# Performance work log

Measured on AMD Instinct MI355X. Metric: run time of the kernel, lower is better.

## Reference

```python
import jax, jax.numpy as jnp
import numpy as np

NUM_GRAPHS = 512
EPS_BN = 1e-5


def _bn(x, g, b):
    # BatchNorm1d in training mode: biased batch statistics over node dim
    m = x.mean(0)
    v = x.var(0)
    return g * (x - m) * jax.lax.rsqrt(v + EPS_BN) + b


def _gcn(x, W, b, src, dst):
    # GCNConv with self-loops and symmetric deg^-1/2 normalization
    n = x.shape[0]
    loop = jnp.arange(n, dtype=src.dtype)
    s = jnp.concatenate([src, loop])
    d = jnp.concatenate([dst, loop])
    h = x @ W  # [N, C_out]
    deg = jax.ops.segment_sum(jnp.ones(d.shape[0], dtype=h.dtype), d, num_segments=n)
    dinv = jax.lax.rsqrt(jnp.maximum(deg, 1.0))  # deg >= 1 due to self-loops
    norm = dinv[s] * dinv[d]  # [E+N]
    out = jax.ops.segment_sum(norm[:, None] * h[s], d, num_segments=n)
    return out + b


def setup_inputs() -> dict:
    key = jax.random.key(0)
    ks = jax.random.split(key, 16)
    N, E, F = 100000, 1600000, 6

    def lin(k, fi, fo):
        k1, k2 = jax.random.split(k)
        s = 1.0 / np.sqrt(fi)
        return (jax.random.uniform(k1, (fi, fo), minval=-s, maxval=s),
                jax.random.uniform(k2, (fo,), minval=-s, maxval=s))

    W1, b1 = lin(ks[0], F, 32)
    W2, b2 = lin(ks[1], 32, 64)
    W3, b3 = lin(ks[2], 64, 128)
    Wf1, bf1 = lin(ks[3], 128, 128)
    Wf2, bf2 = lin(ks[4], 128, 64)
    return {
        "x": jax.random.normal(ks[5], (N, F), dtype=jnp.float32),
        "edge_src": jax.random.randint(ks[6], (E,), 0, N, dtype=jnp.int32),
        "edge_dst": jax.random.randint(ks[7], (E,), 0, N, dtype=jnp.int32),
        "batch": jnp.sort(jax.random.randint(ks[8], (N,), 0, NUM_GRAPHS, dtype=jnp.int32)),
        "W1": W1, "b1": b1, "g1": jnp.ones(32), "be1": jnp.zeros(32),
        "W2": W2, "b2": b2, "g2": jnp.ones(64), "be2": jnp.zeros(64),
        "W3": W3, "b3": b3, "g3": jnp.ones(128), "be3": jnp.zeros(128),
        "Wf1": Wf1, "bf1": bf1, "g4": jnp.ones(128), "be4": jnp.zeros(128),
        "Wf2": Wf2, "bf2": bf2,
    }


def reference(x, edge_src, edge_dst, batch,
              W1, b1, g1, be1, W2, b2, g2, be2, W3, b3, g3, be3,
              Wf1, bf1, g4, be4, Wf2, bf2):
    h = jax.nn.relu(_bn(_gcn(x, W1, b1, edge_src, edge_dst), g1, be1))
    h = jax.nn.relu(_bn(_gcn(h, W2, b2, edge_src, edge_dst), g2, be2))
    h = jax.nn.relu(_bn(_gcn(h, W3, b3, edge_src, edge_dst), g3, be3))
    p = jax.ops.segment_max(h, batch, num_segments=NUM_GRAPHS)  # [G, 128]
    p = jax.nn.relu(_bn(p @ Wf1 + bf1, g4, be4))  # dropout = identity (eval)
    p = p @ Wf2 + bf2
    return p / jnp.maximum(jnp.linalg.norm(p, axis=1, keepdims=True), 1e-12)
```

## Files before the change

kernel.cpp:

```cpp
#include <hip/hip_runtime.h>
#include <hip/hip_bf16.h>
#include <hip/hip_fp16.h>

#define NG 512
#define EPS_BN 1e-5f

typedef unsigned short ushort_t;
typedef unsigned int uint_t;

__device__ __forceinline__ float4 f4add(float4 a, float4 b) {
    a.x += b.x; a.y += b.y; a.z += b.z; a.w += b.w; return a;
}
__device__ __forceinline__ float4 f4fma(float s, float4 b, float4 a) {
    a.x = fmaf(s, b.x, a.x); a.y = fmaf(s, b.y, a.y);
    a.z = fmaf(s, b.z, a.z); a.w = fmaf(s, b.w, a.w); return a;
}
__device__ __forceinline__ float4 f4scale(float s, float4 a) {
    a.x *= s; a.y *= s; a.z *= s; a.w *= s; return a;
}
__device__ __forceinline__ float4 bnrelu4(float4 v, float4 sc, float4 sh) {
    float4 r;
    r.x = fmaxf(fmaf(sc.x, v.x, sh.x), 0.f);
    r.y = fmaxf(fmaf(sc.y, v.y, sh.y), 0.f);
    r.z = fmaxf(fmaf(sc.z, v.z, sh.z), 0.f);
    r.w = fmaxf(fmaf(sc.w, v.w, sh.w), 0.f);
    return r;
}
__device__ __forceinline__ void bnparam(float sm, float sq, float ga, float bt,
                                        float invN, float& sc, float& sh) {
    float m = sm * invN;
    float var = fmaf(-m, m, sq * invN);
    sc = ga * rsqrtf(var + EPS_BN);
    sh = fmaf(-m, sc, bt);
}

__device__ __forceinline__ float4 ldh4(const ushort_t* p) {
    uint2 u = *reinterpret_cast<const uint2*>(p);
    __half2 a = *reinterpret_cast<const __half2*>(&u.x);
    __half2 b = *reinterpret_cast<const __half2*>(&u.y);
    float2 fa = __half22float2(a), fb = __half22float2(b);
    float4 r; r.x = fa.x; r.y = fa.y; r.z = fb.x; r.w = fb.y; return r;
}
__device__ __forceinline__ void sth4(ushort_t* p, float4 v) {
    __half2 a = __float22half2_rn(make_float2(v.x, v.y));
    __half2 b = __float22half2_rn(make_float2(v.z, v.w));
    uint2 u;
    u.x = *reinterpret_cast<uint_t*>(&a);
    u.y = *reinterpret_cast<uint_t*>(&b);
    *reinterpret_cast<uint2*>(p) = u;
}


__global__ void k_count(const int* __restrict__ dst, int* __restrict__ cnt, int E) {
    int i = blockIdx.x * blockDim.x + threadIdx.x;
    if (i < E) atomicAdd(&cnt[dst[i]], 1);
}

__global__ void k_dinv(const int* __restrict__ cnt, float* __restrict__ dinv, int N) {
    int i = blockIdx.x * blockDim.x + threadIdx.x;
    if (i < N) dinv[i] = rsqrtf((float)cnt[i] + 1.0f);
}


#define SCAN_T 256
#define SCAN_I 4

__global__ void k_scan1(const int* __restrict__ in, int* __restrict__ out,
                        int* __restrict__ bsum, int N) {
    __shared__ int lds[SCAN_T];
    int t = threadIdx.x;
    int base = blockIdx.x * (SCAN_T * SCAN_I) + t * SCAN_I;
    int v[SCAN_I];
    int sum = 0;
#pragma unroll
    for (int i = 0; i < SCAN_I; ++i) {
        int idx = base + i;
        v[i] = (idx < N) ? in[idx] : 0;
        sum += v[i];
    }
    lds[t] = sum;
    __syncthreads();
    for (int o = 1; o < SCAN_T; o <<= 1) {
        int a = (t >= o) ? lds[t - o] : 0;
        __syncthreads();
        lds[t] += a;
        __syncthreads();
    }
    int run = lds[t] - sum;
#pragma unroll
    for (int i = 0; i < SCAN_I; ++i) {
        int idx = base + i;
        if (idx < N) out[idx] = run;
        run += v[i];
    }
    if (t == SCAN_T - 1) bsum[blockIdx.x] = lds[SCAN_T - 1];
}

__global__ void k_scan2(int* __restrict__ bs, int nb) {
    __shared__ int lds[SCAN_T];
    int t = threadIdx.x;
    int runbase = 0;
    for (int start = 0; start < nb; start += SCAN_T) {
        int idx = start + t;
        int v = (idx < nb) ? bs[idx] : 0;
        lds[t] = v;
        __syncthreads();
        for (int o = 1; o < SCAN_T; o <<= 1) {
            int a = (t >= o) ? lds[t - o] : 0;
            __syncthreads();
            lds[t] += a;
            __syncthreads();
        }
        if (idx < nb) bs[idx] = runbase + lds[t] - v;
        int tot = lds[SCAN_T - 1];
        __syncthreads();
        runbase += tot;
    }
}

__global__ void k_scan3(int* __restrict__ out, const int* __restrict__ bs, int N) {
    int add = bs[blockIdx.x];
    int base = blockIdx.x * (SCAN_T * SCAN_I) + threadIdx.x * SCAN_I;
#pragma unroll
    for (int i = 0; i < SCAN_I; ++i) {
        int idx = base + i;
        if (idx < N) out[idx] += add;
    }
}


__global__ void k_bucket(const int* __restrict__ src, const int* __restrict__ dst,
                         const float* __restrict__ dinv, const int* __restrict__ rowptr,
                         int* __restrict__ fill, int2* __restrict__ e2, int E) {
    int e = blockIdx.x * blockDim.x + threadIdx.x;
    if (e >= E) return;
    int d = dst[e], s = src[e];
    int pos = rowptr[d] + atomicAdd(&fill[d], 1);
    e2[pos] = make_int2(s, __float_as_int(dinv[s]));
}


template <int COUT>
__global__ __launch_bounds__(256) void k_layer1(
    const int* __restrict__ rowptr, const int* __restrict__ cnt,
    const int2* __restrict__ e2, const float* __restrict__ dinv,
    const float* __restrict__ x, const float* __restrict__ W,
    ushort_t* __restrict__ hout, float* __restrict__ sums,
    float* __restrict__ sumsq, int N) {
    constexpr int NPB = 256;
    constexpr int CG = COUT / 4;
    constexpr int RPB = 256 / CG;
    constexpr int ECAP1 = 4608;
    __shared__ float inT[NPB * 6];
    __shared__ float4 wT[6 * CG];
    __shared__ float4 red[256];
    __shared__ int2 eLDS[ECAP1];
    int t = threadIdx.x;
    const float4* W4 = (const float4*)W;
    for (int i = t; i < 6 * CG; i += 256) wT[i] = W4[i];
    int base = blockIdx.x * NPB;
    int lastn = min(base + NPB, N) - 1;
    int eBeg = rowptr[base];
    int eEnd = rowptr[lastn] + cnt[lastn];
    int M = eEnd - eBeg;
    bool useL = (M <= ECAP1);
    if (useL) {
        for (int i = t; i < M; i += 256) eLDS[i] = e2[eBeg + i];
    }
    __syncthreads();
    {
        const float2* x2 = (const float2*)x;
        int ew = t & 3;
        int nl0 = t >> 2;
#pragma unroll 1
        for (int it = 0; it < 4; ++it) {
            int nl = it * 64 + nl0;
            int n = base + nl;
            float a0 = 0, a1 = 0, a2 = 0, a3 = 0, a4 = 0, a5 = 0;
            float di = 0.f;
            if (n < N) {
                di = dinv[n];
                int beg = rowptr[n], end = beg + cnt[n];
                if (ew == 0) {
                    size_t b3 = (size_t)n * 3;
                    float2 p0 = x2[b3], p1 = x2[b3 + 1], p2 = x2[b3 + 2];
                    a0 = di * p0.x; a1 = di * p0.y; a2 = di * p1.x;
                    a3 = di * p1.y; a4 = di * p2.x; a5 = di * p2.y;
                }
                if (useL) {
                    int r = beg - eBeg + ew, re = end - eBeg;
                    for (; r + 4 < re; r += 8) {
                        int2 pa = eLDS[r], pb = eLDS[r + 4];
                        size_t sa = (size_t)pa.x * 3, sb = (size_t)pb.x * 3;
                        float2 qa0 = x2[sa], qa1 = x2[sa + 1], qa2 = x2[sa + 2];
                        float2 qb0 = x2[sb], qb1 = x2[sb + 1], qb2 = x2[sb + 2];
                        __builtin_amdgcn_sched_barrier(0);
                        float wa = __int_as_float(pa.y), wb = __int_as_float(pb.y);
                        a0 = fmaf(wa, qa0.x, a0); a1 = fmaf(wa, qa0.y, a1);
                        a2 = fmaf(wa, qa1.x, a2); a3 = fmaf(wa, qa1.y, a3);
                        a4 = fmaf(wa, qa2.x, a4); a5 = fmaf(wa, qa2.y, a5);
                        a0 = fmaf(wb, qb0.x, a0); a1 = fmaf(wb, qb0.y, a1);
                        a2 = fmaf(wb, qb1.x, a2); a3 = fmaf(wb, qb1.y, a3);
                        a4 = fmaf(wb, qb2.x, a4); a5 = fmaf(wb, qb2.y, a5);
                    }
                    if (r < re) {
                        int2 pa = eLDS[r];
                        size_t sa = (size_t)pa.x * 3;
                        float2 qa0 = x2[sa], qa1 = x2[sa + 1], qa2 = x2[sa + 2];
                        float wa = __int_as_float(pa.y);
                        a0 = fmaf(wa, qa0.x, a0); a1 = fmaf(wa, qa0.y, a1);
                        a2 = fmaf(wa, qa1.x, a2); a3 = fmaf(wa, qa1.y, a3);
                        a4 = fmaf(wa, qa2.x, a4); a5 = fmaf(wa, qa2.y, a5);
                    }
                } else {
                    for (int e = beg + ew; e < end; e += 4) {
                        int2 pa = e2[e];
                        size_t sa = (size_t)pa.x * 3;
                        float2 qa0 = x2[sa], qa1 = x2[sa + 1], qa2 = x2[sa + 2];
                        float wa = __int_as_float(pa.y);
                        a0 = fmaf(wa, qa0.x, a0); a1 = fmaf(wa, qa0.y, a1);
                        a2 = fmaf(wa, qa1.x, a2); a3 = fmaf(wa, qa1.y, a3);
                        a4 = fmaf(wa, qa2.x, a4); a5 = fmaf(wa, qa2.y, a5);
                    }
                }
            }
#pragma unroll
            for (int m = 1; m < 4; m <<= 1) {
                a0 += __shfl_xor(a0, m); a1 += __shfl_xor(a1, m);
                a2 += __shfl_xor(a2, m); a3 += __shfl_xor(a3, m);
                a4 += __shfl_xor(a4, m); a5 += __shfl_xor(a5, m);
            }
            if (ew == 0 && n < N) {
                int o = nl * 6;
                inT[o + 0] = di * a0; inT[o + 1] = di * a1; inT[o + 2] = di * a2;
                inT[o + 3] = di * a3; inT[o + 4] = di * a4; inT[o + 5] = di * a5;
            }
        }
    }
    __syncthreads();
    int gi = t % CG, r0 = t / CG, c0 = gi * 4;
    int nrows = min(NPB, N - base);
    float4 s = {0, 0, 0, 0}, s2 = {0, 0, 0, 0};
    for (int r = r0; r < nrows; r += RPB) {
        const float* row = inT + r * 6;
        float4 acc = {0, 0, 0, 0};
#pragma unroll
        for (int k = 0; k < 6; ++k) acc = f4fma(row[k], wT[k * CG + gi], acc);
        sth4(hout + (size_t)(base + r) * COUT + gi * 4, acc);
        s = f4add(s, acc);
        s2.x = fmaf(acc.x, acc.x, s2.x);
        s2.y = fmaf(acc.y, acc.y, s2.y);
        s2.z = fmaf(acc.z, acc.z, s2.z);
        s2.w = fmaf(acc.w, acc.w, s2.w);
    }
    red[t] = s;
    for (int hh = RPB / 2; hh > 0; hh >>= 1) {
        __syncthreads();
        if (r0 < hh) red[t] = f4add(red[t], red[t + hh * CG]);
    }
    if (r0 == 0) {
        float4 a = red[t];
        atomicAdd(&sums[c0 + 0], a.x); atomicAdd(&sums[c0 + 1], a.y);
        atomicAdd(&sums[c0 + 2], a.z); atomicAdd(&sums[c0 + 3], a.w);
    }
    __syncthreads();
    red[t] = s2;
    for (int hh = RPB / 2; hh > 0; hh >>= 1) {
        __syncthreads();
        if (r0 < hh) red[t] = f4add(red[t], red[t + hh * CG]);
    }
    if (r0 == 0) {
        float4 b = red[t];
        atomicAdd(&sumsq[c0 + 0], b.x); atomicAdd(&sumsq[c0 + 1], b.y);
        atomicAdd(&sumsq[c0 + 2], b.z); atomicAdd(&sumsq[c0 + 3], b.w);
    }
}


template <int CIN, int COUT, int NPB>
__global__ __launch_bounds__(256, 4) void k_layer(
    const int* __restrict__ rowptr, const int* __restrict__ cnt,
    const int2* __restrict__ e2, const float* __restrict__ dinv,
    const ushort_t* __restrict__ hin,
    const float* __restrict__ sums_in, const float* __restrict__ sumsq_in,
    const float* __restrict__ gam, const float* __restrict__ bet,
    const float* __restrict__ W, ushort_t* __restrict__ hout,
    float* __restrict__ sums_out, float* __restrict__ sumsq_out,
    int N, float invN) {
    constexpr int TPN = CIN / 4;
    constexpr int PAD = TPN + 1;
    constexpr int ITER1 = NPB * TPN / 256;
    constexpr int NPI = 256 / TPN;
    constexpr int CG = COUT / 4;
    constexpr int RPB = 256 / CG;
    constexpr int ECAP = 2048;
    __shared__ float4 inT4[NPB * PAD];
    __shared__ float4 red[256];
    __shared__ int2 eLDS[ECAP];
    int t = threadIdx.x;
    const float4* W4 = (const float4*)W;
    int base = blockIdx.x * NPB;
    int lastn = min(base + NPB, N) - 1;
    int eBeg = rowptr[base];
    int eEnd = rowptr[lastn] + cnt[lastn];
    int M = eEnd - eBeg;
    bool useL = (M <= ECAP);
    if (useL) {
        for (int i = t; i < M; i += 256) eLDS[i] = e2[eBeg + i];
    }
    __syncthreads();
    {
        int c4 = t % TPN;
        float4 sm = reinterpret_cast<const float4*>(sums_in)[c4];
        float4 sq = reinterpret_cast<const float4*>(sumsq_in)[c4];
        float4 ga = reinterpret_cast<const float4*>(gam)[c4];
        float4 bt = reinterpret_cast<const float4*>(bet)[c4];
        float4 sc, sh;
        bnparam(sm.x, sq.x, ga.x, bt.x, invN, sc.x, sh.x);
        bnparam(sm.y, sq.y, ga.y, bt.y, invN, sc.y, sh.y);
        bnparam(sm.z, sq.z, ga.z, bt.z, invN, sc.z, sh.z);
        bnparam(sm.w, sq.w, ga.w, bt.w, invN, sc.w, sh.w);
        const ushort_t* hu = hin;
        int co = c4 * 4;
#pragma unroll
        for (int it = 0; it < ITER1; ++it) {
            int nl = it * NPI + t / TPN;
            int n = base + nl;
            if (n < N) {
                int beg = rowptr[n], end = beg + cnt[n];
                float di = dinv[n];
                float4 acc = f4scale(di, bnrelu4(ldh4(hu + (size_t)n * CIN + co), sc, sh));
                if (useL) {
                    int r = beg - eBeg, re = end - eBeg;
                    for (; r + 7 < re; r += 8) {
                        int2 p0 = eLDS[r],     p1 = eLDS[r + 1];
                        int2 p2_ = eLDS[r + 2], p3_ = eLDS[r + 3];
                        int2 p4 = eLDS[r + 4], p5 = eLDS[r + 5];
                        int2 p6 = eLDS[r + 6], p7 = eLDS[r + 7];
                        float4 v0 = ldh4(hu + (size_t)p0.x * CIN + co);
                        float4 v1 = ldh4(hu + (size_t)p1.x * CIN + co);
                        float4 v2 = ldh4(hu + (size_t)p2_.x * CIN + co);
                        float4 v3 = ldh4(hu + (size_t)p3_.x * CIN + co);
                        float4 v4 = ldh4(hu + (size_t)p4.x * CIN + co);
                        float4 v5 = ldh4(hu + (size_t)p5.x * CIN + co);
                        float4 v6 = ldh4(hu + (size_t)p6.x * CIN + co);
                        float4 v7 = ldh4(hu + (size_t)p7.x * CIN + co);
                        __builtin_amdgcn_sched_barrier(0);
                        acc = f4fma(__int_as_float(p0.y), bnrelu4(v0, sc, sh), acc);
                        acc = f4fma(__int_as_float(p1.y), bnrelu4(v1, sc, sh), acc);
                        acc = f4fma(__int_as_float(p2_.y), bnrelu4(v2, sc, sh), acc);
                        acc = f4fma(__int_as_float(p3_.y), bnrelu4(v3, sc, sh), acc);
                        acc = f4fma(__int_as_float(p4.y), bnrelu4(v4, sc, sh), acc);
                        acc = f4fma(__int_as_float(p5.y), bnrelu4(v5, sc, sh), acc);
                        acc = f4fma(__int_as_float(p6.y), bnrelu4(v6, sc, sh), acc);
                        acc = f4fma(__int_as_float(p7.y), bnrelu4(v7, sc, sh), acc);
                    }
                    for (; r + 3 < re; r += 4) {
                        int2 p0 = eLDS[r], p1 = eLDS[r + 1];
                        int2 p2_ = eLDS[r + 2], p3_ = eLDS[r + 3];
                        float4 v0 = ldh4(hu + (size_t)p0.x * CIN + co);
                        float4 v1 = ldh4(hu + (size_t)p1.x * CIN + co);
                        float4 v2 = ldh4(hu + (size_t)p2_.x * CIN + co);
                        float4 v3 = ldh4(hu + (size_t)p3_.x * CIN + co);
                        __builtin_amdgcn_sched_barrier(0);
                        acc = f4fma(__int_as_float(p0.y), bnrelu4(v0, sc, sh), acc);
                        acc = f4fma(__int_as_float(p1.y), bnrelu4(v1, sc, sh), acc);
                        acc = f4fma(__int_as_float(p2_.y), bnrelu4(v2, sc, sh), acc);
                        acc = f4fma(__int_as_float(p3_.y), bnrelu4(v3, sc, sh), acc);
                    }
                    for (; r < re; ++r) {
                        int2 p0 = eLDS[r];
                        acc = f4fma(__int_as_float(p0.y),
                                    bnrelu4(ldh4(hu + (size_t)p0.x * CIN + co), sc, sh), acc);
                    }
                } else {
                    for (int e = beg; e < end; ++e) {
                        int2 p0 = e2[e];
                        acc = f4fma(__int_as_float(p0.y),
                                    bnrelu4(ldh4(hu + (size_t)p0.x * CIN + co), sc, sh), acc);
                    }
                }
                inT4[nl * PAD + c4] = f4scale(di, acc);
            }
        }
    }
    __syncthreads();
    int gi = t % CG, r0 = t / CG, c0 = gi * 4;
    int nrows = min(NPB, N - base);
    float4 s = {0, 0, 0, 0}, s2 = {0, 0, 0, 0};
    for (int r = r0; r < nrows; r += RPB) {
        const float* row = (const float*)(inT4 + r * PAD);
        float4 acc = {0, 0, 0, 0};
#pragma unroll 8
        for (int k = 0; k < CIN; ++k) acc = f4fma(row[k], W4[k * CG + gi], acc);
        sth4(hout + (size_t)(base + r) * COUT + gi * 4, acc);
        s = f4add(s, acc);
        s2.x = fmaf(acc.x, acc.x, s2.x);
        s2.y = fmaf(acc.y, acc.y, s2.y);
        s2.z = fmaf(acc.z, acc.z, s2.z);
        s2.w = fmaf(acc.w, acc.w, s2.w);
    }
    red[t] = s;
    for (int hh = RPB / 2; hh > 0; hh >>= 1) {
        __syncthreads();
        if (r0 < hh) red[t] = f4add(red[t], red[t + hh * CG]);
    }
    if (r0 == 0) {
        float4 a = red[t];
        atomicAdd(&sums_out[c0 + 0], a.x); atomicAdd(&sums_out[c0 + 1], a.y);
        atomicAdd(&sums_out[c0 + 2], a.z); atomicAdd(&sums_out[c0 + 3], a.w);
    }
    __syncthreads();
    red[t] = s2;
    for (int hh = RPB / 2; hh > 0; hh >>= 1) {
        __syncthreads();
        if (r0 < hh) red[t] = f4add(red[t], red[t + hh * CG]);
    }
    if (r0 == 0) {
        float4 b = red[t];
        atomicAdd(&sumsq_out[c0 + 0], b.x); atomicAdd(&sumsq_out[c0 + 1], b.y);
        atomicAdd(&sumsq_out[c0 + 2], b.z); atomicAdd(&sumsq_out[c0 + 3], b.w);
    }
}


template <int CIN, int COUT, int ROWS>
__global__ __launch_bounds__(256) void k_mm_stats(
    const float* __restrict__ in, const float* __restrict__ W,
    float* __restrict__ out, float* __restrict__ sums,
    float* __restrict__ sumsq, int N) {
    constexpr int CG = COUT / 4;
    constexpr int RPB = 256 / CG;
    __shared__ float4 inT4[ROWS * CIN / 4];
    float* inT = (float*)inT4;
    __shared__ float4 wT[CIN * CG];
    __shared__ float4 red[256];
    int t = threadIdx.x;
    const float4* W4 = reinterpret_cast<const float4*>(W);
    for (int i = t; i < CIN * CG; i += 256) wT[i] = W4[i];
    int base = blockIdx.x * ROWS;
    int nrows = min(ROWS, N - base);
    {
        const float4* in4 = reinterpret_cast<const float4*>(in + (size_t)base * CIN);
        int tot = nrows * (CIN / 4);
        for (int i = t; i < tot; i += 256) inT4[i] = in4[i];
    }
    __syncthreads();
    int gi = t % CG, r0 = t / CG, c0 = gi * 4;
    float4 s = {0, 0, 0, 0}, s2 = {0, 0, 0, 0};
    for (int r = r0; r < nrows; r += RPB) {
        const float* row = inT + r * CIN;
        float4 acc = {0, 0, 0, 0};
#pragma unroll
        for (int k = 0; k < CIN; ++k) acc = f4fma(row[k], wT[k * CG + gi], acc);
        reinterpret_cast<float4*>(out + (size_t)(base + r) * COUT)[gi] = acc;
        s = f4add(s, acc);
        s2.x = fmaf(acc.x, acc.x, s2.x);
        s2.y = fmaf(acc.y, acc.y, s2.y);
        s2.z = fmaf(acc.z, acc.z, s2.z);
        s2.w = fmaf(acc.w, acc.w, s2.w);
    }
    red[t] = s;
    for (int hh = RPB / 2; hh > 0; hh >>= 1) {
        __syncthreads();
        if (r0 < hh) red[t] = f4add(red[t], red[t + hh * CG]);
    }
    if (r0 == 0) {
        float4 a = red[t];
        atomicAdd(&sums[c0 + 0], a.x); atomicAdd(&sums[c0 + 1], a.y);
        atomicAdd(&sums[c0 + 2], a.z); atomicAdd(&sums[c0 + 3], a.w);
    }
    __syncthreads();
    red[t] = s2;
    for (int hh = RPB / 2; hh > 0; hh >>= 1) {
        __syncthreads();
        if (r0 < hh) red[t] = f4add(red[t], red[t + hh * CG]);
    }
    if (r0 == 0) {
        float4 b = red[t];
        atomicAdd(&sumsq[c0 + 0], b.x); atomicAdd(&sumsq[c0 + 1], b.y);
        atomicAdd(&sumsq[c0 + 2], b.z); atomicAdd(&sumsq[c0 + 3], b.w);
    }
}


__global__ void k_segmax_bn(const ushort_t* __restrict__ h, const int* __restrict__ batch,
                            const float* __restrict__ sums, const float* __restrict__ sumsq,
                            const float* __restrict__ gam, const float* __restrict__ bet,
                            float* __restrict__ pool, int N, float invN) {
    int t = threadIdx.x;
    int c = t & 127;
    int sub = t >> 7;
    int base = blockIdx.x * 64 + sub * 32;
    if (base >= N) return;
    float sc, sh;
    bnparam(sums[c], sumsq[c], gam[c], bet[c], invN, sc, sh);
    int cur = batch[base];
    float h0 = __half2float(*reinterpret_cast<const __half*>(&h[(size_t)base * 128 + c]));
    float mx = fmaxf(fmaf(sc, h0, sh), 0.f);
    int lim = min(32, N - base);
    for (int i = 1; i < lim; ++i) {
        int n = base + i;
        int b = batch[n];
        float hv = __half2float(*reinterpret_cast<const __half*>(&h[(size_t)n * 128 + c]));
        float v = fmaxf(fmaf(sc, hv, sh), 0.f);
        if (b != cur) {
            atomicMax(reinterpret_cast<int*>(pool) + (cur << 7) + c, __float_as_int(mx));
            cur = b; mx = v;
        } else {
            mx = fmaxf(mx, v);
        }
    }
    atomicMax(reinterpret_cast<int*>(pool) + (cur << 7) + c, __float_as_int(mx));
}


__global__ void k_head(const float* __restrict__ Z, const float* __restrict__ sums,
                       const float* __restrict__ sumsq, const float* __restrict__ gam,
                       const float* __restrict__ bet, const float* __restrict__ Wf2,
                       const float* __restrict__ bf2, float* __restrict__ out) {
    int g = blockIdx.x, c = threadIdx.x;
    __shared__ float row[128];
    const float invG = 1.0f / (float)NG;
    for (int j = c; j < 128; j += 64) {
        float sc, sh;
        bnparam(sums[j], sumsq[j], gam[j], bet[j], invG, sc, sh);
        row[j] = fmaxf(fmaf(sc, Z[(g << 7) + j], sh), 0.f);
    }
    __syncthreads();
    float acc = bf2[c];
#pragma unroll
    for (int k = 0; k < 128; ++k) acc = fmaf(row[k], Wf2[k * 64 + c], acc);
    float ss = acc * acc;
#pragma unroll
    for (int off = 32; off; off >>= 1) ss += __shfl_xor(ss, off);
    out[(g << 6) + c] = acc / fmaxf(sqrtf(ss), 1e-12f);
}


extern "C" void kernel_launch(void* const* d_in, const int* in_sizes, int n_in,
                              void* d_out, int out_size, void* d_ws, size_t ws_size,
                              hipStream_t stream) {
    const float* x    = (const float*)d_in[0];
    const int*   src  = (const int*)d_in[1];
    const int*   dst  = (const int*)d_in[2];
    const int*   batch= (const int*)d_in[3];
    const float* W1   = (const float*)d_in[4];
    const float* g1   = (const float*)d_in[6];
    const float* be1  = (const float*)d_in[7];
    const float* W2   = (const float*)d_in[8];
    const float* g2   = (const float*)d_in[10];
    const float* be2  = (const float*)d_in[11];
    const float* W3   = (const float*)d_in[12];
    const float* g3   = (const float*)d_in[14];
    const float* be3  = (const float*)d_in[15];
    const float* Wf1  = (const float*)d_in[16];
    const float* g4   = (const float*)d_in[18];
    const float* be4  = (const float*)d_in[19];
    const float* Wf2  = (const float*)d_in[20];
    const float* bf2  = (const float*)d_in[21];
    float* out = (float*)d_out;

    const int N = in_sizes[0] / 6;
    const int E = in_sizes[1];
    const int nScanBlocks = (N + SCAN_T * SCAN_I - 1) / (SCAN_T * SCAN_I);

    char* ws = (char*)d_ws;
    size_t off = 0;
    auto carve = [&](size_t bytes) {
        void* p = ws + off;
        off += (bytes + 255) & ~(size_t)255;
        return p;
    };
    int*     cnt    = (int*)carve((size_t)N * 4);
    float*   dinv   = (float*)carve((size_t)N * 4);
    int*     rowptr = (int*)carve((size_t)N * 4);
    int*     fill   = (int*)carve((size_t)N * 4);
    int*     bsum   = (int*)carve((size_t)4096 * 4);
    int2*    e2     = (int2*)carve((size_t)E * 8);
    ushort_t* H1    = (ushort_t*)carve((size_t)N * 32 * 2);
    ushort_t* H2    = (ushort_t*)carve((size_t)N * 64 * 2);
    ushort_t* H3    = (ushort_t*)carve((size_t)N * 128 * 2);
    float*   stats  = (float*)carve(704 * 4);
    float*   pool   = (float*)carve((size_t)NG * 128 * 4);
    float*   Z      = (float*)carve((size_t)NG * 128 * 4);
    float* s1 = stats;
    float* s2 = stats + 64;
    float* s3 = stats + 192;
    float* s4 = stats + 448;

    const float invN = 1.0f / (float)N;

    hipMemsetAsync(cnt, 0, (size_t)N * 4, stream);
    hipMemsetAsync(fill, 0, (size_t)N * 4, stream);
    hipMemsetAsync(stats, 0, 704 * 4, stream);
    hipMemsetAsync(pool, 0, (size_t)NG * 128 * 4, stream);
    k_count<<<(E + 255) / 256, 256, 0, stream>>>(dst, cnt, E);
    k_dinv<<<(N + 255) / 256, 256, 0, stream>>>(cnt, dinv, N);
    k_scan1<<<nScanBlocks, SCAN_T, 0, stream>>>(cnt, rowptr, bsum, N);
    k_scan2<<<1, SCAN_T, 0, stream>>>(bsum, nScanBlocks);
    k_scan3<<<nScanBlocks, SCAN_T, 0, stream>>>(rowptr, bsum, N);
    k_bucket<<<(E + 255) / 256, 256, 0, stream>>>(src, dst, dinv, rowptr, fill, e2, E);

    k_layer1<32><<<(N + 255) / 256, 256, 0, stream>>>(
        rowptr, cnt, e2, dinv, x, W1, H1, s1, s1 + 32, N);

    k_layer<32, 64, 64><<<(N + 63) / 64, 256, 0, stream>>>(
        rowptr, cnt, e2, dinv, H1, s1, s1 + 32, g1, be1, W2, H2,
        s2, s2 + 64, N, invN);

    k_layer<64, 128, 64><<<(N + 63) / 64, 256, 0, stream>>>(
        rowptr, cnt, e2, dinv, H2, s2, s2 + 64, g2, be2, W3, H3,
        s3, s3 + 128, N, invN);

    k_segmax_bn<<<(N + 63) / 64, 256, 0, stream>>>(H3, batch, s3, s3 + 128, g3, be3, pool, N, invN);

    k_mm_stats<128, 128, 64><<<(NG + 63) / 64, 256, 0, stream>>>(pool, Wf1, Z, s4, s4 + 128, NG);
    k_head<<<NG, 64, 0, stream>>>(Z, s4, s4 + 128, g4, be4, Wf2, bf2, out);
}
```

Measured before the change: 751.5 us.

## Store hidden features in column-sliced planes and gather one slice at a time

Layer outputs are now written as column slices of 16 channels (layers 1 and 2) instead of full interleaved rows. The next layer's aggregation loops over these slices, so each gather pass reads 32-byte rows from a smaller plane that fits better in cache, rather than scattered 64/128-byte rows. The cost is that the edge list is walked several times per block (ISPLIT passes), with more loop overhead and more index loads. Layer 3 keeps its full-row output layout, so the downstream segmax reads the same layout as before.

```diff
diff --git a/kernel.cpp b/kernel.cpp
--- a/kernel.cpp
+++ b/kernel.cpp
@@ -241,12 +241,13 @@
     int gi = t % CG, r0 = t / CG, c0 = gi * 4;
     int nrows = min(NPB, N - base);
     float4 s = {0, 0, 0, 0}, s2 = {0, 0, 0, 0};
+    size_t hoff = (size_t)(c0 / 16) * (size_t)N * 16 + (size_t)(c0 % 16);
     for (int r = r0; r < nrows; r += RPB) {
         const float* row = inT + r * 6;
         float4 acc = {0, 0, 0, 0};
 #pragma unroll
         for (int k = 0; k < 6; ++k) acc = f4fma(row[k], wT[k * CG + gi], acc);
-        sth4(hout + (size_t)(base + r) * COUT + gi * 4, acc);
+        sth4(hout + hoff + (size_t)(base + r) * 16, acc);
         s = f4add(s, acc);
         s2.x = fmaf(acc.x, acc.x, s2.x);
         s2.y = fmaf(acc.y, acc.y, s2.y);
@@ -277,7 +278,7 @@
 }
 
 
-template <int CIN, int COUT, int NPB>
+template <int CIN, int COUT, int NPB, int ISPLIT, int OSPLIT>
 __global__ __launch_bounds__(256, 4) void k_layer(
     const int* __restrict__ rowptr, const int* __restrict__ cnt,
     const int2* __restrict__ e2, const float* __restrict__ dinv,
@@ -287,12 +288,14 @@
     const float* __restrict__ W, ushort_t* __restrict__ hout,
     float* __restrict__ sums_out, float* __restrict__ sumsq_out,
     int N, float invN) {
-    constexpr int TPN = CIN / 4;
-    constexpr int PAD = TPN + 1;
-    constexpr int ITER1 = NPB * TPN / 256;
+    constexpr int CINP = CIN / ISPLIT;
+    constexpr int TPN = CINP / 4;
+    constexpr int PAD = CIN / 4 + 1;
     constexpr int NPI = 256 / TPN;
+    constexpr int ITERP = NPB * TPN / 256;
     constexpr int CG = COUT / 4;
     constexpr int RPB = 256 / CG;
+    constexpr int CPSO = COUT / OSPLIT;
     constexpr int ECAP = 2048;
     __shared__ float4 inT4[NPB * PAD];
     __shared__ float4 red[256];
@@ -311,76 +314,80 @@
     __syncthreads();
     {
         int c4 = t % TPN;
-        float4 sm = reinterpret_cast<const float4*>(sums_in)[c4];
-        float4 sq = reinterpret_cast<const float4*>(sumsq_in)[c4];
-        float4 ga = reinterpret_cast<const float4*>(gam)[c4];
-        float4 bt = reinterpret_cast<const float4*>(bet)[c4];
-        float4 sc, sh;
-        bnparam(sm.x, sq.x, ga.x, bt.x, invN, sc.x, sh.x);
-        bnparam(sm.y, sq.y, ga.y, bt.y, invN, sc.y, sh.y);
-        bnparam(sm.z, sq.z, ga.z, bt.z, invN, sc.z, sh.z);
-        bnparam(sm.w, sq.w, ga.w, bt.w, invN, sc.w, sh.w);
-        const ushort_t* hu = hin;
         int co = c4 * 4;
-#pragma unroll
-        for (int it = 0; it < ITER1; ++it) {
-            int nl = it * NPI + t / TPN;
-            int n = base + nl;
-            if (n < N) {
-                int beg = rowptr[n], end = beg + cnt[n];
-                float di = dinv[n];
-                float4 acc = f4scale(di, bnrelu4(ldh4(hu + (size_t)n * CIN + co), sc, sh));
-                if (useL) {
-                    int r = beg - eBeg, re = end - eBeg;
-                    for (; r + 7 < re; r += 8) {
-                        int2 p0 = eLDS[r],     p1 = eLDS[r + 1];
-                        int2 p2_ = eLDS[r + 2], p3_ = eLDS[r + 3];
-                        int2 p4 = eLDS[r + 4], p5 = eLDS[r + 5];
-                        int2 p6 = eLDS[r + 6], p7 = eLDS[r + 7];
-                        float4 v0 = ldh4(hu + (size_t)p0.x * CIN + co);
-                        float4 v1 = ldh4(hu + (size_t)p1.x * CIN + co);
-                        float4 v2 = ldh4(hu + (size_t)p2_.x * CIN + co);
-                        float4 v3 = ldh4(hu + (size_t)p3_.x * CIN + co);
-                        float4 v4 = ldh4(hu + (size_t)p4.x * CIN + co);
-                        float4 v5 = ldh4(hu + (size_t)p5.x * CIN + co);
-                        float4 v6 = ldh4(hu + (size_t)p6.x * CIN + co);
-                        float4 v7 = ldh4(hu + (size_t)p7.x * CIN + co);
-                        __builtin_amdgcn_sched_barrier(0);
-                        acc = f4fma(__int_as_float(p0.y), bnrelu4(v0, sc, sh), acc);
-                        acc = f4fma(__int_as_float(p1.y), bnrelu4(v1, sc, sh), acc);
-                        acc = f4fma(__int_as_float(p2_.y), bnrelu4(v2, sc, sh), acc);
-                        acc = f4fma(__int_as_float(p3_.y), bnrelu4(v3, sc, sh), acc);
-                        acc = f4fma(__int_as_float(p4.y), bnrelu4(v4, sc, sh), acc);
-                        acc = f4fma(__int_as_float(p5.y), bnrelu4(v5, sc, sh), acc);
-                        acc = f4fma(__int_as_float(p6.y), bnrelu4(v6, sc, sh), acc);
-                        acc = f4fma(__int_as_float(p7.y), bnrelu4(v7, sc, sh), acc);
+#pragma unroll 1
+        for (int sp = 0; sp < ISPLIT; ++sp) {
+            int gc4 = sp * TPN + c4;
+            float4 sm = reinterpret_cast<const float4*>(sums_in)[gc4];
+            float4 sq = reinterpret_cast<const float4*>(sumsq_in)[gc4];
+            float4 ga = reinterpret_cast<const float4*>(gam)[gc4];
+            float4 bt = reinterpret_cast<const float4*>(bet)[gc4];
+            float4 sc, sh;
+            bnparam(sm.x, sq.x, ga.x, bt.x, invN, sc.x, sh.x);
+            bnparam(sm.y, sq.y, ga.y, bt.y, invN, sc.y, sh.y);
+            bnparam(sm.z, sq.z, ga.z, bt.z, invN, sc.z, sh.z);
+            bnparam(sm.w, sq.w, ga.w, bt.w, invN, sc.w, sh.w);
+            const ushort_t* hsp = hin + (size_t)sp * (size_t)N * CINP;
+#pragma unroll
+            for (int it = 0; it < ITERP; ++it) {
+                int nl = it * NPI + t / TPN;
+                int n = base + nl;
+                if (n < N) {
+                    int beg = rowptr[n], end = beg + cnt[n];
+                    float di = dinv[n];
+                    float4 acc = f4scale(di, bnrelu4(ldh4(hsp + (size_t)n * CINP + co), sc, sh));
+                    if (useL) {
+                        int r = beg - eBeg, re = end - eBeg;
+                        for (; r + 7 < re; r += 8) {
+                            int2 p0 = eLDS[r],     p1 = eLDS[r + 1];
+                            int2 p2_ = eLDS[r + 2], p3_ = eLDS[r + 3];
+                            int2 p4 = eLDS[r + 4], p5 = eLDS[r + 5];
+                            int2 p6 = eLDS[r + 6], p7 = eLDS[r + 7];
+                            float4 v0 = ldh4(hsp + (size_t)p0.x * CINP + co);
+                            float4 v1 = ldh4(hsp + (size_t)p1.x * CINP + co);
+                            float4 v2 = ldh4(hsp + (size_t)p2_.x * CINP + co);
+                            float4 v3 = ldh4(hsp + (size_t)p3_.x * CINP + co);
+                            float4 v4 = ldh4(hsp + (size_t)p4.x * CINP + co);
+                            float4 v5 = ldh4(hsp + (size_t)p5.x * CINP + co);
+                            float4 v6 = ldh4(hsp + (size_t)p6.x * CINP + co);
+                            float4 v7 = ldh4(hsp + (size_t)p7.x * CINP + co);
+                            __builtin_amdgcn_sched_barrier(0);
+                            acc = f4fma(__int_as_float(p0.y), bnrelu4(v0, sc, sh), acc);
+                            acc = f4fma(__int_as_float(p1.y), bnrelu4(v1, sc, sh), acc);
+                            acc = f4fma(__int_as_float(p2_.y), bnrelu4(v2, sc, sh), acc);
+                            acc = f4fma(__int_as_float(p3_.y), bnrelu4(v3, sc, sh), acc);
+                            acc = f4fma(__int_as_float(p4.y), bnrelu4(v4, sc, sh), acc);
+                            acc = f4fma(__int_as_float(p5.y), bnrelu4(v5, sc, sh), acc);
+                            acc = f4fma(__int_as_float(p6.y), bnrelu4(v6, sc, sh), acc);
+                            acc = f4fma(__int_as_float(p7.y), bnrelu4(v7, sc, sh), acc);
+                        }
+                        for (; r + 3 < re; r += 4) {
+                            int2 p0 = eLDS[r], p1 = eLDS[r + 1];
+                            int2 p2_ = eLDS[r + 2], p3_ = eLDS[r + 3];
+                            float4 v0 = ldh4(hsp + (size_t)p0.x * CINP + co);
+                            float4 v1 = ldh4(hsp + (size_t)p1.x * CINP + co);
+                            float4 v2 = ldh4(hsp + (size_t)p2_.x * CINP + co);
+                            float4 v3 = ldh4(hsp + (size_t)p3_.x * CINP + co);
+                            __builtin_amdgcn_sched_barrier(0);
+                            acc = f4fma(__int_as_float(p0.y), bnrelu4(v0, sc, sh), acc);
+                            acc = f4fma(__int_as_float(p1.y), bnrelu4(v1, sc, sh), acc);
+                            acc = f4fma(__int_as_float(p2_.y), bnrelu4(v2, sc, sh), acc);
+                            acc = f4fma(__int_as_float(p3_.y), bnrelu4(v3, sc, sh), acc);
+                        }
+                        for (; r < re; ++r) {
+                            int2 p0 = eLDS[r];
+                            acc = f4fma(__int_as_float(p0.y),
+                                        bnrelu4(ldh4(hsp + (size_t)p0.x * CINP + co), sc, sh), acc);
+                        }
+                    } else {
+                        for (int e = beg; e < end; ++e) {
+                            int2 p0 = e2[e];
+                            acc = f4fma(__int_as_float(p0.y),
+                                        bnrelu4(ldh4(hsp + (size_t)p0.x * CINP + co), sc, sh), acc);
+                        }
                     }
-                    for (; r + 3 < re; r += 4) {
-                        int2 p0 = eLDS[r], p1 = eLDS[r + 1];
-                        int2 p2_ = eLDS[r + 2], p3_ = eLDS[r + 3];
-                        float4 v0 = ldh4(hu + (size_t)p0.x * CIN + co);
-                        float4 v1 = ldh4(hu + (size_t)p1.x * CIN + co);
-                        float4 v2 = ldh4(hu + (size_t)p2_.x * CIN + co);
-                        float4 v3 = ldh4(hu + (size_t)p3_.x * CIN + co);
-                        __builtin_amdgcn_sched_barrier(0);
-                        acc = f4fma(__int_as_float(p0.y), bnrelu4(v0, sc, sh), acc);
-                        acc = f4fma(__int_as_float(p1.y), bnrelu4(v1, sc, sh), acc);
-                        acc = f4fma(__int_as_float(p2_.y), bnrelu4(v2, sc, sh), acc);
-                        acc = f4fma(__int_as_float(p3_.y), bnrelu4(v3, sc, sh), acc);
-                    }
-                    for (; r < re; ++r) {
-                        int2 p0 = eLDS[r];
-                        acc = f4fma(__int_as_float(p0.y),
-                                    bnrelu4(ldh4(hu + (size_t)p0.x * CIN + co), sc, sh), acc);
-                    }
-                } else {
-                    for (int e = beg; e < end; ++e) {
-                        int2 p0 = e2[e];
-                        acc = f4fma(__int_as_float(p0.y),
-                                    bnrelu4(ldh4(hu + (size_t)p0.x * CIN + co), sc, sh), acc);
-                    }
+                    inT4[nl * PAD + sp * TPN + c4] = f4scale(di, acc);
                 }
-                inT4[nl * PAD + c4] = f4scale(di, acc);
             }
         }
     }
@@ -388,12 +395,13 @@
     int gi = t % CG, r0 = t / CG, c0 = gi * 4;
     int nrows = min(NPB, N - base);
     float4 s = {0, 0, 0, 0}, s2 = {0, 0, 0, 0};
+    size_t hoff = (size_t)(c0 / CPSO) * (size_t)N * CPSO + (size_t)(c0 % CPSO);
     for (int r = r0; r < nrows; r += RPB) {
         const float* row = (const float*)(inT4 + r * PAD);
         float4 acc = {0, 0, 0, 0};
 #pragma unroll 8
         for (int k = 0; k < CIN; ++k) acc = f4fma(row[k], W4[k * CG + gi], acc);
-        sth4(hout + (size_t)(base + r) * COUT + gi * 4, acc);
+        sth4(hout + hoff + (size_t)(base + r) * CPSO, acc);
         s = f4add(s, acc);
         s2.x = fmaf(acc.x, acc.x, s2.x);
         s2.y = fmaf(acc.y, acc.y, s2.y);
@@ -605,11 +613,11 @@
     k_layer1<32><<<(N + 255) / 256, 256, 0, stream>>>(
         rowptr, cnt, e2, dinv, x, W1, H1, s1, s1 + 32, N);
 
-    k_layer<32, 64, 64><<<(N + 63) / 64, 256, 0, stream>>>(
+    k_layer<32, 64, 64, 2, 4><<<(N + 63) / 64, 256, 0, stream>>>(
         rowptr, cnt, e2, dinv, H1, s1, s1 + 32, g1, be1, W2, H2,
         s2, s2 + 64, N, invN);
 
-    k_layer<64, 128, 64><<<(N + 63) / 64, 256, 0, stream>>>(
+    k_layer<64, 128, 64, 4, 1><<<(N + 63) / 64, 256, 0, stream>>>(
         rowptr, cnt, e2, dinv, H2, s2, s2 + 64, g2, be2, W3, H3,
         s3, s3 + 128, N, invN);
 
```

Result: slower. 776.6 us (+3.3%).
